# Optimization experiments

Measured on AMD Instinct MI355X. Metric: run time of the kernel, lower is better.

Reference implementation:

```python
import jax, jax.numpy as jnp
import numpy as np
import itertools

# --- constants matching init_kwargs / chosen problem size ---
MOD = 6.283185307179586       # 2*pi, modular wrap for angular error
DEG_U = 90.0                  # deg_u
DEG_P = 1.0                   # deg_p (grid resolution in degrees)
D = 4                         # number of active sources (ones per label row)
NUM_CLASSES = 181             # angle grid size
BATCH = 131072

# All D! permutations as one-hot matrices: exact LAP solution by brute force
# (equivalent to lap.lapjv on the square DxD cost matrix).
_PERMS = np.array(list(itertools.permutations(range(D))), dtype=np.int32)   # (D!, D)
PERM_OH = jnp.asarray(np.eye(D, dtype=np.float32)[_PERMS])                  # (D!, D, D)


def setup_inputs() -> dict:
    key = jax.random.key(0)
    k1, k2 = jax.random.split(key)
    # predicted DOAs live in the first D slots of logits (radians)
    logits = jax.random.normal(k1, (BATCH, NUM_CLASSES), dtype=jnp.float32)
    # labels: exactly D ones per row (D distinct grid indices)
    scores = jax.random.uniform(k2, (BATCH, NUM_CLASSES))
    idx = jnp.argsort(scores, axis=1)[:, :D]                     # D distinct cols per row
    labels = jnp.zeros((BATCH, NUM_CLASSES), dtype=jnp.int32)
    labels = labels.at[jnp.arange(BATCH)[:, None], idx].set(1)
    return {"logits": logits, "labels": labels}


def _sq_mod_diff(a, b):
    # ((a - b + mod/2) % mod - mod/2)**2 : squared wrapped angular error
    d = jnp.mod(a - b + MOD / 2, MOD) - MOD / 2
    return d * d


def reference(logits, labels):
    # np.where(labels==1)[0] returns ascending indices of the ones.
    # Stable ascending argsort of a 0/1 row puts the one-indices (in ascending
    # order) in the last D slots.
    one_idx = jnp.argsort(labels, axis=1)[:, -D:]                        # (B, D)
    label_ang = (one_idx.astype(jnp.float32) * DEG_P - DEG_U) * (jnp.pi / 180.0)  # (B, D) radians

    doa = logits[:, :D]                                                  # (B, D)
    # per-sample DxD cost matrix of squared modular errors
    cost = _sq_mod_diff(doa[:, :, None], label_ang[:, None, :])          # (B, D, D)
    # optimal assignment = min total cost over all permutations (exact LAP)
    totals = jnp.einsum('bij,pij->bp', cost, PERM_OH)                    # (B, D!)
    min_total = jnp.min(totals, axis=1)                                  # (B,)
    rmse = jnp.sqrt(min_total / D)                                       # (B,)
    return rmse.mean()
```

## Files before the change

kernel.cpp:

```cpp
#include <hip/hip_runtime.h>
#include <hip/hip_bf16.h>
#include <math.h>

constexpr int   NC      = 181;
constexpr int   BATCH   = 131072;
constexpr float MODC    = 6.2831853071795864769f;
constexpr float HALFMOD = 3.1415926535897932385f;
constexpr float DEG2RAD = 0.017453292519943295f;

constexpr unsigned MAGIC181 = 23729102u;

constexpr int RPB   = 256;
constexpr int WINT4 = RPB * NC / 4;
constexpr int NPT   = WINT4 / 1024;
constexpr int REM   = WINT4 - NPT * 1024;

__device__ __forceinline__ float sq_mod_diff(float x) {
    float t = x + HALFMOD;
    float m = t - floorf(t * (1.0f / MODC)) * MODC;
    float d = m - HALFMOD;
    return d * d;
}

__device__ __forceinline__ void deposit(unsigned g, unsigned rowBase,
                                        unsigned* __restrict__ bm) {
    const unsigned row  = __umulhi(g, MAGIC181);
    const unsigned cls  = g - 181u * row;
    const unsigned lrow = row - rowBase;
    atomicOr(&bm[lrow * 8u + (cls >> 5u)], 1u << (cls & 31u));
}

__global__ __launch_bounds__(1024) void fused_kernel(
    const float* __restrict__ logits,
    const int*   __restrict__ labels,
    float*       __restrict__ out)
{
    __shared__ unsigned bm[RPB * 8];
    __shared__ float    wsum[4];

    const int tid = threadIdx.x;
    const unsigned rowBase = blockIdx.x * RPB;

    bm[tid]        = 0u;
    bm[tid + 1024] = 0u;
    __syncthreads();

    const unsigned base4 = (unsigned)blockIdx.x * WINT4 + tid;
    const int4* p4 = (const int4*)labels;
    int4 v[NPT + 1];
    #pragma unroll
    for (int k = 0; k < NPT; ++k)
        v[k] = p4[(size_t)base4 + (size_t)k * 1024];
    {
        int4 t = {0, 0, 0, 0};
        if (tid < REM) t = p4[(size_t)base4 + (size_t)NPT * 1024];
        v[NPT] = t;
    }

    float d0 = 0.f, d1 = 0.f, d2 = 0.f, d3 = 0.f;
    if (tid < RPB) {
        const float* lp = logits + (size_t)(rowBase + tid) * NC;
        d0 = lp[0]; d1 = lp[1]; d2 = lp[2]; d3 = lp[3];
    }

    #pragma unroll
    for (int k = 0; k < NPT + 1; ++k) {
        const int4 w = v[k];
        if ((w.x | w.y | w.z | w.w) != 0) {
            const unsigned g0 = (base4 + (unsigned)k * 1024u) * 4u;
            if (w.x != 0) deposit(g0 + 0u, rowBase, bm);
            if (w.y != 0) deposit(g0 + 1u, rowBase, bm);
            if (w.z != 0) deposit(g0 + 2u, rowBase, bm);
            if (w.w != 0) deposit(g0 + 3u, rowBase, bm);
        }
    }
    __syncthreads();

    float sum = 0.0f;
    if (tid < RPB) {
        const float doa[4] = {d0, d1, d2, d3};

        float ang[4];
        int found = 0;
        #pragma unroll
        for (int k = 0; k < 8; ++k) {
            unsigned mm = bm[tid * 8 + k];
            while (mm) {
                const int j = __builtin_ctz(mm);
                mm &= mm - 1;
                ang[found & 3] = ((float)(k * 32 + j) - 90.0f) * DEG2RAD;
                ++found;
            }
        }

        float cst[4][4];
        #pragma unroll
        for (int i = 0; i < 4; ++i)
            #pragma unroll
            for (int j = 0; j < 4; ++j)
                cst[i][j] = sq_mod_diff(doa[i] - ang[j]);

        float best = 1e30f;
        #pragma unroll
        for (int a = 0; a < 4; ++a) {
            #pragma unroll
            for (int b = 0; b < 4; ++b) {
                if (b == a) continue;
                const float top = cst[0][a] + cst[1][b];
                #pragma unroll
                for (int e = 0; e < 4; ++e) {
                    if (e == a || e == b) continue;
                    const int f = 6 - a - b - e;
                    best = fminf(best, top + cst[2][e] + cst[3][f]);
                }
            }
        }
        sum = sqrtf(best * 0.25f);

        #pragma unroll
        for (int off = 32; off > 0; off >>= 1)
            sum += __shfl_down(sum, off);
        if ((tid & 63) == 0) wsum[tid >> 6] = sum;
    }
    __syncthreads();

    if (tid == 0) {
        const float t = (wsum[0] + wsum[1]) + (wsum[2] + wsum[3]);
        atomicAdd(out, t * (1.0f / (float)BATCH));
    }
}

extern "C" void kernel_launch(void* const* d_in, const int* in_sizes, int n_in,
                              void* d_out, int out_size, void* d_ws, size_t ws_size,
                              hipStream_t stream) {
    const float* logits = (const float*)d_in[0];
    const int*   labels = (const int*)d_in[1];
    float*       out    = (float*)d_out;

    hipMemsetAsync(out, 0, sizeof(float), stream);

    fused_kernel<<<BATCH / RPB, 1024, 0, stream>>>(logits, labels, out);
}
```

Measured before the change: 194.1 us.

## Stage label tiles into LDS via direct global-to-LDS loads with smaller blocks

Blocks now handle 64 rows with 256 threads. The label window is copied straight into shared memory with global_load_lds 16-byte loads, then scanned from LDS to set the bitmask bits. The final reduction drops the cross-wave shared sum and issues one atomicAdd per block, since only one wave computes rows. The goal is more blocks in flight and loads issued without register staging, at the cost of extra LDS traffic and four times as many global atomics.

```diff
diff --git a/kernel.cpp b/kernel.cpp
--- a/kernel.cpp
+++ b/kernel.cpp
@@ -10,10 +10,10 @@
 
 constexpr unsigned MAGIC181 = 23729102u;
 
-constexpr int RPB   = 256;
+constexpr int RPB   = 64;
 constexpr int WINT4 = RPB * NC / 4;
-constexpr int NPT   = WINT4 / 1024;
-constexpr int REM   = WINT4 - NPT * 1024;
+constexpr int NOPS  = (WINT4 + 63) / 64;
+constexpr int OPW   = (NOPS + 3) / 4;
 
 __device__ __forceinline__ float sq_mod_diff(float x) {
     float t = x + HALFMOD;
@@ -22,40 +22,21 @@
     return d * d;
 }
 
-__device__ __forceinline__ void deposit(unsigned g, unsigned rowBase,
-                                        unsigned* __restrict__ bm) {
-    const unsigned row  = __umulhi(g, MAGIC181);
-    const unsigned cls  = g - 181u * row;
-    const unsigned lrow = row - rowBase;
-    atomicOr(&bm[lrow * 8u + (cls >> 5u)], 1u << (cls & 31u));
-}
-
-__global__ __launch_bounds__(1024) void fused_kernel(
+__global__ __launch_bounds__(256) void fused_kernel(
     const float* __restrict__ logits,
     const int*   __restrict__ labels,
     float*       __restrict__ out)
 {
+    __shared__ int4     win[WINT4];
     __shared__ unsigned bm[RPB * 8];
-    __shared__ float    wsum[4];
 
-    const int tid = threadIdx.x;
-    const unsigned rowBase = blockIdx.x * RPB;
+    const int tid  = threadIdx.x;
+    const int lane = tid & 63;
+    const int w    = tid >> 6;
+    const int rowBase = blockIdx.x * RPB;
 
-    bm[tid]        = 0u;
-    bm[tid + 1024] = 0u;
-    __syncthreads();
-
-    const unsigned base4 = (unsigned)blockIdx.x * WINT4 + tid;
-    const int4* p4 = (const int4*)labels;
-    int4 v[NPT + 1];
-    #pragma unroll
-    for (int k = 0; k < NPT; ++k)
-        v[k] = p4[(size_t)base4 + (size_t)k * 1024];
-    {
-        int4 t = {0, 0, 0, 0};
-        if (tid < REM) t = p4[(size_t)base4 + (size_t)NPT * 1024];
-        v[NPT] = t;
-    }
+    bm[tid]       = 0u;
+    bm[tid + 256] = 0u;
 
     float d0 = 0.f, d1 = 0.f, d2 = 0.f, d3 = 0.f;
     if (tid < RPB) {
@@ -63,20 +44,46 @@
         d0 = lp[0]; d1 = lp[1]; d2 = lp[2]; d3 = lp[3];
     }
 
+    const int4* gbase = (const int4*)labels + (size_t)blockIdx.x * WINT4;
     #pragma unroll
-    for (int k = 0; k < NPT + 1; ++k) {
-        const int4 w = v[k];
-        if ((w.x | w.y | w.z | w.w) != 0) {
-            const unsigned g0 = (base4 + (unsigned)k * 1024u) * 4u;
-            if (w.x != 0) deposit(g0 + 0u, rowBase, bm);
-            if (w.y != 0) deposit(g0 + 1u, rowBase, bm);
-            if (w.z != 0) deposit(g0 + 2u, rowBase, bm);
-            if (w.w != 0) deposit(g0 + 3u, rowBase, bm);
+    for (int k = 0; k < OPW; ++k) {
+        const int op = w * OPW + k;
+        if (op < NOPS) {
+            const int x4 = op * 64 + lane;
+            if (x4 < WINT4) {
+                __builtin_amdgcn_global_load_lds(
+                    (const __attribute__((address_space(1))) void*)(gbase + x4),
+                    (__attribute__((address_space(3))) void*)(&win[x4]),
+                    16, 0, 0);
+            }
         }
     }
     __syncthreads();
 
-    float sum = 0.0f;
+    #pragma unroll
+    for (int k = 0; k < OPW; ++k) {
+        const int idx = tid + 256 * k;
+        if (idx < WINT4) {
+            const int4 v = win[idx];
+            if ((v.x | v.y | v.z | v.w) != 0) {
+                const unsigned g0 = (unsigned)idx * 4u;
+                #pragma unroll
+                for (int c = 0; c < 4; ++c) {
+                    const int comp = (c == 0) ? v.x : (c == 1) ? v.y
+                                   : (c == 2) ? v.z : v.w;
+                    if (comp != 0) {
+                        const unsigned g   = g0 + (unsigned)c;
+                        const unsigned row = __umulhi(g, MAGIC181);
+                        const unsigned cls = g - 181u * row;
+                        atomicOr(&bm[row * 8u + (cls >> 5u)],
+                                 1u << (cls & 31u));
+                    }
+                }
+            }
+        }
+    }
+    __syncthreads();
+
     if (tid < RPB) {
         const float doa[4] = {d0, d1, d2, d3};
 
@@ -115,18 +122,13 @@
                 }
             }
         }
-        sum = sqrtf(best * 0.25f);
+        float sum = sqrtf(best * 0.25f);
 
         #pragma unroll
         for (int off = 32; off > 0; off >>= 1)
             sum += __shfl_down(sum, off);
-        if ((tid & 63) == 0) wsum[tid >> 6] = sum;
-    }
-    __syncthreads();
-
-    if (tid == 0) {
-        const float t = (wsum[0] + wsum[1]) + (wsum[2] + wsum[3]);
-        atomicAdd(out, t * (1.0f / (float)BATCH));
+        if (lane == 0)
+            atomicAdd(out, sum * (1.0f / (float)BATCH));
     }
 }
 
@@ -139,5 +141,5 @@
 
     hipMemsetAsync(out, 0, sizeof(float), stream);
 
-    fused_kernel<<<BATCH / RPB, 1024, 0, stream>>>(logits, labels, out);
+    fused_kernel<<<BATCH / RPB, 256, 0, stream>>>(logits, labels, out);
 }
```

Measured after the change: 194.3 us. About the same (+0.1%).
